# Optimization experiments

Hardware: AMD Instinct MI355X
Metric: run time of the kernel (lower is better)

The kernel has to match this reference:

```python
import jax, jax.numpy as jnp
import numpy as np

TEMPERATURE = 0.07
NEG = -1e9  # finite stand-in for -inf; exp(-1e9) underflows to 0 in fp32, identical math


def setup_inputs() -> dict:
    key = jax.random.key(0)
    k1, k2 = jax.random.split(key)
    B, D = 8192, 128
    emb = jax.random.normal(k1, (B, D), dtype=jnp.float32)
    emb = emb / jnp.linalg.norm(emb, axis=1, keepdims=True)  # docstring: normalized embeddings
    labels = jax.random.randint(k2, (B,), 0, 2048, dtype=jnp.int64)
    return {"embeddings": emb, "labels": labels}


def reference(embeddings, labels):
    B = labels.shape[0]
    # [B, B] pairwise similarities / temperature
    sim = jnp.matmul(embeddings, embeddings.T) / TEMPERATURE
    eye = jnp.eye(B, dtype=bool)
    sim = jnp.where(eye, NEG, sim)  # mask self-similarity
    # positives: same outfit id, excluding self
    pos_mask = (labels[None, :] == labels[:, None]) & (~eye)
    # row-wise log-softmax (torch code does log_softmax over each row)
    log_probs = jax.nn.log_softmax(sim, axis=1)
    pos_count = jnp.sum(pos_mask, axis=1)  # [B]
    pos_sum = jnp.sum(jnp.where(pos_mask, log_probs, 0.0), axis=1)  # [B]
    has_pos = pos_count > 0
    row_mean = jnp.where(has_pos, pos_sum / jnp.maximum(pos_count, 1), 0.0)
    count = jnp.sum(has_pos)
    loss = -jnp.sum(row_mean) / jnp.maximum(count, 1)
    return loss
```

## Files before the change

### kernel.cpp

```cpp
#include <hip/hip_runtime.h>


#define BATCH 8192
#define DIMK  128
#define INV_T 14.285714285714286f
#define MSUB  14.285714285714286f
#define K1    20.609929155311264f
#define K2    20.609929155311264f

typedef short bf16x8 __attribute__((ext_vector_type(8)));
typedef float f32x4  __attribute__((ext_vector_type(4)));

__device__ __forceinline__ unsigned short f2bf_rne(float f) {
    unsigned u = __float_as_uint(f);
    u += 0x7FFFu + ((u >> 16) & 1u);
    return (unsigned short)(u >> 16);
}
__device__ __forceinline__ float bf2f(unsigned short b) {
    return __uint_as_float(((unsigned)b) << 16);
}

__global__ __launch_bounds__(256) void
prep_kernel(const float* __restrict__ emb, const int* __restrict__ labels,
            ushort* __restrict__ Ebf, float* __restrict__ gsum, int* __restrict__ gcnt,
            float4* __restrict__ zcol4) {
    if (blockIdx.x < 1024) {
        int i = blockIdx.x * 256 + threadIdx.x;
        if (i < 2048) {
            float4 z = {0.f, 0.f, 0.f, 0.f};
            zcol4[i] = z;
        }
        float4 v = ((const float4*)emb)[i];
        ushort4 o;
        o.x = f2bf_rne(v.x); o.y = f2bf_rne(v.y);
        o.z = f2bf_rne(v.z); o.w = f2bf_rne(v.w);
        ((ushort4*)Ebf)[i] = o;
    } else {
        __shared__ int labs[BATCH];
        const int tid = threadIdx.x;
#pragma unroll
        for (int it = 0; it < 8; ++it)
            ((int4*)labs)[it * 256 + tid] = ((const int4*)labels)[it * 256 + tid];
        __syncthreads();

        const int lane = tid & 63;
        const int wid  = tid >> 6;
        const int c    = (blockIdx.x - 1024) * 4 + wid;
        float2 acc = {0.f, 0.f};
        int cnt = 0;
        int nl = labs[lane];
        for (int j0 = 0; j0 < BATCH; j0 += 64) {
            int cur = nl;
            int nidx = j0 + 64 < BATCH ? j0 + 64 : 0;
            nl = labs[nidx + lane];
            unsigned long long m = __ballot(cur == c);
            cnt += __popcll(m);
            while (m) {
                int j = __ffsll(m) - 1;
                m &= m - 1;
                float2 v = *(const float2*)(emb + (size_t)(j0 + j) * DIMK + lane * 2);
                acc.x += v.x; acc.y += v.y;
            }
        }
        *(float2*)(gsum + (size_t)c * DIMK + lane * 2) = acc;
        if (lane == 0) gcnt[c] = cnt;
    }
}

__global__ __launch_bounds__(512) void
contrastive_main(const ushort* __restrict__ Ebf, float* __restrict__ zpartR,
                 float* __restrict__ zcol) {
    __shared__ __align__(16) ushort Bs[2048 * 8];
    __shared__ float cpart[8][128];
    const int tid  = threadIdx.x;
    const int lane = tid & 63;
    const int wid  = tid >> 6;
    const int quad = lane >> 4;
    const int l16  = lane & 15;

    int b = blockIdx.x >> 1;
    const int ch = blockIdx.x & 1;
    int ti = 0;
    while (b >= 32 - ti) { b -= 32 - ti; ++ti; }
    const int tj  = ti + b;
    const int tj2 = tj * 2 + ch;
    const int row_base = ti * 256 + wid * 32;
    const int col_base = tj * 256 + ch * 128;

    bf16x8 afrag[2][4];
#pragma unroll
    for (int mt = 0; mt < 2; ++mt)
#pragma unroll
        for (int kk = 0; kk < 4; ++kk)
            afrag[mt][kk] = *(const bf16x8*)(Ebf + (size_t)(row_base + mt * 16 + l16) * DIMK
                                             + kk * 32 + quad * 8);

#pragma unroll
    for (int it = 0; it < 4; ++it) {
        int f   = it * 512 + tid;
        int col = f >> 4;
        int c   = f & 15;
        uint4 v = *(const uint4*)(Ebf + (size_t)(col_base + col) * DIMK + c * 8);
        *(uint4*)&Bs[((col >> 4) * 256 + c * 16 + ((col & 15) ^ c)) * 8] = v;
    }
    __syncthreads();

    float zacc[8];
#pragma unroll
    for (int s = 0; s < 8; ++s) zacc[s] = 0.f;

    for (int nt = 0; nt < 8; ++nt) {
        bf16x8 bfrag[4];
#pragma unroll
        for (int kk = 0; kk < 4; ++kk) {
            const int c2 = kk * 4 + quad;
            bfrag[kk] = *(const bf16x8*)&Bs[(nt * 256 + c2 * 16 + (l16 ^ c2)) * 8];
        }

        float csum = 0.f;
#pragma unroll
        for (int mt = 0; mt < 2; ++mt) {
            f32x4 c = {0.f, 0.f, 0.f, 0.f};
#pragma unroll
            for (int kk = 0; kk < 4; ++kk)
                c = __builtin_amdgcn_mfma_f32_16x16x32_bf16(afrag[mt][kk], bfrag[kk], c, 0, 0, 0);
#pragma unroll
            for (int r = 0; r < 4; ++r) {
                float e = __builtin_amdgcn_exp2f(__builtin_fmaf(c[r], K1, -K2));
                zacc[mt * 4 + r] += e;
                csum += e;
            }
        }
        csum += __shfl_xor(csum, 16, 64);
        csum += __shfl_xor(csum, 32, 64);
        if (quad == 0) cpart[wid][nt * 16 + l16] = csum;
    }

#pragma unroll
    for (int s = 0; s < 8; ++s) {
        float z = zacc[s];
#pragma unroll
        for (int m = 1; m <= 8; m <<= 1) z += __shfl_xor(z, m, 64);
        if (l16 == 0) {
            int row = row_base + (s >> 2) * 16 + quad * 4 + (s & 3);
            zpartR[(size_t)tj2 * BATCH + row] = z;
        }
    }

    __syncthreads();
    if (ti != tj && tid < 128) {
        float s = cpart[0][tid] + cpart[1][tid] + cpart[2][tid] + cpart[3][tid]
                + cpart[4][tid] + cpart[5][tid] + cpart[6][tid] + cpart[7][tid];
        atomicAdd(&zcol[col_base + tid], s);
    }
}

__global__ __launch_bounds__(256) void
finalize1(const float* __restrict__ emb, const ushort* __restrict__ Ebf,
          const int* __restrict__ labels, const float* __restrict__ gsum,
          const int* __restrict__ gcnt, const float* __restrict__ zpartR,
          const float* __restrict__ zcol,
          float* __restrict__ bpart, int* __restrict__ bcnt) {
    __shared__ float sf[4];
    __shared__ int   si[4];
    const int lane = threadIdx.x & 63;
    const int wid  = threadIdx.x >> 6;

    float wsum = 0.f;
    int   wcnt = 0;
#pragma unroll
    for (int it = 0; it < 4; ++it) {
        const int r   = blockIdx.x * 16 + wid * 4 + it;
        const int lab = labels[r];
        const int P   = gcnt[lab] - 1;
        const int tp2 = (r >> 8) * 2;

        float2 ev = *(const float2*)(emb  + (size_t)r   * DIMK + lane * 2);
        float2 gv = *(const float2*)(gsum + (size_t)lab * DIMK + lane * 2);
        unsigned bb = *(const unsigned*)(Ebf + (size_t)r * DIMK + lane * 2);
        float b0 = bf2f((unsigned short)(bb & 0xFFFF));
        float b1 = bf2f((unsigned short)(bb >> 16));

        float dotg = ev.x * gv.x + ev.y * gv.y;
        float ssd  = ev.x * ev.x + ev.y * ev.y;
        float sdbf = b0 * b0 + b1 * b1;
        float Z = 0.f;
        if (lane >= tp2) Z = zpartR[(size_t)lane * BATCH + r];

#pragma unroll
        for (int m = 1; m <= 32; m <<= 1) {
            dotg += __shfl_xor(dotg, m, 64);
            ssd  += __shfl_xor(ssd,  m, 64);
            sdbf += __shfl_xor(sdbf, m, 64);
            Z    += __shfl_xor(Z,    m, 64);
        }
        Z += zcol[r];
        Z -= __builtin_amdgcn_exp2f(__builtin_fmaf(sdbf, K1, -K2));

        const bool has = (P > 0);
        wsum += has ? ((dotg - ssd) * INV_T / (float)P - MSUB - __logf(Z)) : 0.f;
        wcnt += has ? 1 : 0;
    }

    if (lane == 0) { sf[wid] = wsum; si[wid] = wcnt; }
    __syncthreads();
    if (threadIdx.x == 0) {
        bpart[blockIdx.x] = sf[0] + sf[1] + sf[2] + sf[3];
        bcnt [blockIdx.x] = si[0] + si[1] + si[2] + si[3];
    }
}

__global__ __launch_bounds__(256) void
finalize2(const float* __restrict__ bpart, const int* __restrict__ bcnt,
          float* __restrict__ out) {
    __shared__ float sf[4];
    __shared__ int   si[4];
    const int t = threadIdx.x;
    float v = 0.f; int c = 0;
#pragma unroll
    for (int k = 0; k < 2; ++k) {
        v += bpart[t + k * 256];
        c += bcnt [t + k * 256];
    }
#pragma unroll
    for (int m = 1; m <= 32; m <<= 1) {
        v += __shfl_xor(v, m, 64);
        c += __shfl_xor(c, m, 64);
    }
    if ((t & 63) == 0) { sf[t >> 6] = v; si[t >> 6] = c; }
    __syncthreads();
    if (t == 0) {
        float tot = sf[0] + sf[1] + sf[2] + sf[3];
        int cc = si[0] + si[1] + si[2] + si[3];
        out[0] = -tot / (float)(cc > 0 ? cc : 1);
    }
}

extern "C" void kernel_launch(void* const* d_in, const int* in_sizes, int n_in,
                              void* d_out, int out_size, void* d_ws, size_t ws_size,
                              hipStream_t stream) {
    const float* emb  = (const float*)d_in[0];
    const int* labels = (const int*)d_in[1];
    float* out        = (float*)d_out;

    char* ws = (char*)d_ws;
    ushort* Ebf    = (ushort*)ws;
    float*  zpartR = (float*)(ws + (2u << 20));
    float*  zcol   = (float*)(ws + (4u << 20));
    float*  gsum   = (float*)(ws + (5u << 20));
    int*    gcnt   = (int*)  (ws + (6u << 20));
    float*  bpart  = (float*)(ws + (6u << 20) + 8192);
    int*    bcnt   = (int*)  (ws + (6u << 20) + 16384);

    prep_kernel<<<1536, 256, 0, stream>>>(emb, labels, Ebf, gsum, gcnt,
                                          (float4*)zcol);
    contrastive_main<<<1056, 512, 0, stream>>>(Ebf, zpartR, zcol);
    finalize1<<<512, 256, 0, stream>>>(emb, Ebf, labels, gsum, gcnt, zpartR, zcol,
                                       bpart, bcnt);
    finalize2<<<1, 256, 0, stream>>>(bpart, bcnt, out);
}
```

Measured before the change: 96.65 us.

## Move label group-sum work into main GEMM kernel and remap tile order

The per-label embedding sum and count computation moves out of the prep kernel into extra blocks appended to the main similarity kernel, so it runs alongside the exp-sum tiles instead of in front of them. These blocks reuse the tile shared buffer for labels and now handle 8 labels per block. Tile blocks are renumbered with an XCD-style swizzle that spreads consecutive block ids across groups. The partial row-sum buffer is also transposed to row-major [row][64] so finalize1 reads it contiguously. The risk is that the long-running label-scan blocks land at the end of the grid and become a tail.

```diff
diff --git a/kernel.cpp b/kernel.cpp
--- a/kernel.cpp
+++ b/kernel.cpp
@@ -21,31 +21,41 @@
 }
 
 __global__ __launch_bounds__(256) void
-prep_kernel(const float* __restrict__ emb, const int* __restrict__ labels,
-            ushort* __restrict__ Ebf, float* __restrict__ gsum, int* __restrict__ gcnt,
+prep_kernel(const float* __restrict__ emb, ushort* __restrict__ Ebf,
             float4* __restrict__ zcol4) {
-    if (blockIdx.x < 1024) {
-        int i = blockIdx.x * 256 + threadIdx.x;
-        if (i < 2048) {
-            float4 z = {0.f, 0.f, 0.f, 0.f};
-            zcol4[i] = z;
-        }
-        float4 v = ((const float4*)emb)[i];
-        ushort4 o;
-        o.x = f2bf_rne(v.x); o.y = f2bf_rne(v.y);
-        o.z = f2bf_rne(v.z); o.w = f2bf_rne(v.w);
-        ((ushort4*)Ebf)[i] = o;
-    } else {
-        __shared__ int labs[BATCH];
-        const int tid = threadIdx.x;
-#pragma unroll
-        for (int it = 0; it < 8; ++it)
-            ((int4*)labs)[it * 256 + tid] = ((const int4*)labels)[it * 256 + tid];
+    int i = blockIdx.x * 256 + threadIdx.x;
+    if (i < 2048) {
+        float4 z = {0.f, 0.f, 0.f, 0.f};
+        zcol4[i] = z;
+    }
+    float4 v = ((const float4*)emb)[i];
+    ushort4 o;
+    o.x = f2bf_rne(v.x); o.y = f2bf_rne(v.y);
+    o.z = f2bf_rne(v.z); o.w = f2bf_rne(v.w);
+    ((ushort4*)Ebf)[i] = o;
+}
+
+__global__ __launch_bounds__(512) void
+contrastive_main(const ushort* __restrict__ Ebf, float* __restrict__ zpartR,
+                 float* __restrict__ zcol, const float* __restrict__ emb,
+                 const int* __restrict__ labels, float* __restrict__ gsum,
+                 int* __restrict__ gcnt) {
+    __shared__ __align__(16) ushort Bs[2048 * 8];
+    __shared__ float cpart[8][128];
+    const int tid  = threadIdx.x;
+    const int lane = tid & 63;
+    const int wid  = tid >> 6;
+    const int quad = lane >> 4;
+    const int l16  = lane & 15;
+
+    if (blockIdx.x >= 1056) {
+        int* labs = (int*)&Bs[0];
+#pragma unroll
+        for (int it = 0; it < 4; ++it)
+            ((int4*)labs)[it * 512 + tid] = ((const int4*)labels)[it * 512 + tid];
         __syncthreads();
 
-        const int lane = tid & 63;
-        const int wid  = tid >> 6;
-        const int c    = (blockIdx.x - 1024) * 4 + wid;
+        const int c = (blockIdx.x - 1056) * 8 + wid;
         float2 acc = {0.f, 0.f};
         int cnt = 0;
         int nl = labs[lane];
@@ -64,22 +74,14 @@
         }
         *(float2*)(gsum + (size_t)c * DIMK + lane * 2) = acc;
         if (lane == 0) gcnt[c] = cnt;
-    }
-}
-
-__global__ __launch_bounds__(512) void
-contrastive_main(const ushort* __restrict__ Ebf, float* __restrict__ zpartR,
-                 float* __restrict__ zcol) {
-    __shared__ __align__(16) ushort Bs[2048 * 8];
-    __shared__ float cpart[8][128];
-    const int tid  = threadIdx.x;
-    const int lane = tid & 63;
-    const int wid  = tid >> 6;
-    const int quad = lane >> 4;
-    const int l16  = lane & 15;
-
-    int b = blockIdx.x >> 1;
-    const int ch = blockIdx.x & 1;
+        return;
+    }
+
+    const int bid = blockIdx.x;
+    const int tt  = (bid & 7) * 132 + (bid >> 3);
+
+    int b = tt >> 1;
+    const int ch = tt & 1;
     int ti = 0;
     while (b >= 32 - ti) { b -= 32 - ti; ++ti; }
     const int tj  = ti + b;
@@ -143,7 +145,7 @@
         for (int m = 1; m <= 8; m <<= 1) z += __shfl_xor(z, m, 64);
         if (l16 == 0) {
             int row = row_base + (s >> 2) * 16 + quad * 4 + (s & 3);
-            zpartR[(size_t)tj2 * BATCH + row] = z;
+            zpartR[(size_t)row * 64 + tj2] = z;
         }
     }
 
@@ -185,7 +187,7 @@
         float ssd  = ev.x * ev.x + ev.y * ev.y;
         float sdbf = b0 * b0 + b1 * b1;
         float Z = 0.f;
-        if (lane >= tp2) Z = zpartR[(size_t)lane * BATCH + r];
+        if (lane >= tp2) Z = zpartR[(size_t)r * 64 + lane];
 
 #pragma unroll
         for (int m = 1; m <= 32; m <<= 1) {
@@ -252,9 +254,9 @@
     float*  bpart  = (float*)(ws + (6u << 20) + 8192);
     int*    bcnt   = (int*)  (ws + (6u << 20) + 16384);
 
-    prep_kernel<<<1536, 256, 0, stream>>>(emb, labels, Ebf, gsum, gcnt,
-                                          (float4*)zcol);
-    contrastive_main<<<1056, 512, 0, stream>>>(Ebf, zpartR, zcol);
+    prep_kernel<<<1024, 256, 0, stream>>>(emb, Ebf, (float4*)zcol);
+    contrastive_main<<<1312, 512, 0, stream>>>(Ebf, zpartR, zcol,
+                                               emb, labels, gsum, gcnt);
     finalize1<<<512, 256, 0, stream>>>(emb, Ebf, labels, gsum, gcnt, zpartR, zcol,
                                        bpart, bcnt);
     finalize2<<<1, 256, 0, stream>>>(bpart, bcnt, out);
```

New measurement: 93.28 us. -3.5%, faster.
